# Kernel tuning notes

Hardware: AMD Instinct MI355X
Metric: run time of the kernel (lower is better)

The kernel has to match this reference:

```python
import jax, jax.numpy as jnp
import numpy as np

SCALE = 4
D_MODEL = 128   # in_channels // scale
D_STATE = 16
D_CONV = 4
D_INNER = 256   # expand * d_model
DT_RANK = 8     # ceil(d_model / 16)


def setup_inputs() -> dict:
    key = jax.random.key(0)
    ks = jax.random.split(key, 10)
    B, C, H, W = 4, 512, 48, 48
    s = 0.02
    x = jax.random.normal(ks[0], (B, C, H, W), jnp.float32)
    in_proj_w = jax.random.normal(ks[1], (SCALE, 2 * D_INNER, D_MODEL), jnp.float32) * s
    conv_w = jax.random.normal(ks[2], (SCALE, D_INNER, D_CONV), jnp.float32) * s
    conv_b = jax.random.normal(ks[3], (SCALE, D_INNER), jnp.float32) * s
    x_proj_w = jax.random.normal(ks[4], (SCALE, DT_RANK + 2 * D_STATE, D_INNER), jnp.float32) * s
    dt_proj_w = jax.random.normal(ks[5], (SCALE, D_INNER, DT_RANK), jnp.float32) * s
    dt_proj_b = jax.random.uniform(ks[6], (SCALE, D_INNER), jnp.float32, 0.001, 0.1)
    A_log = jnp.broadcast_to(jnp.log(jnp.arange(1, D_STATE + 1, dtype=jnp.float32)), (SCALE, D_INNER, D_STATE)).copy()
    D = jnp.ones((SCALE, D_INNER), jnp.float32)
    out_proj_w = jax.random.normal(ks[7], (SCALE, D_MODEL, D_INNER), jnp.float32) * s
    return {"x": x, "in_proj_w": in_proj_w, "conv_w": conv_w, "conv_b": conv_b,
            "x_proj_w": x_proj_w, "dt_proj_w": dt_proj_w, "dt_proj_b": dt_proj_b,
            "A_log": A_log, "D": D, "out_proj_w": out_proj_w}


def _mamba(u, Wi, wc, bc, Wx, Wdt, bdt, A_log, Dp, Wo):
    # u: (B, L, d_model)
    B, L, _ = u.shape
    di, n, dtr, dc = Wo.shape[1], A_log.shape[1], Wdt.shape[1], wc.shape[1]
    xz = u @ Wi.T                                   # (B, L, 2*di)
    xp, z = jnp.split(xz, 2, axis=-1)
    # causal depthwise conv along L
    xc = jax.lax.conv_general_dilated(xp.transpose(0, 2, 1), wc[:, None, :], (1,),
                                      [(dc - 1, 0)], feature_group_count=di)
    xs = jax.nn.silu(xc + bc[None, :, None]).transpose(0, 2, 1)  # (B, L, di)
    dbc = xs @ Wx.T
    dt, Bm, Cm = dbc[..., :dtr], dbc[..., dtr:dtr + n], dbc[..., dtr + n:]
    delta = jax.nn.softplus(dt @ Wdt.T + bdt)       # (B, L, di)
    A = -jnp.exp(A_log)                             # (di, n)
    dA = jnp.exp(jnp.einsum('bld,dn->bldn', delta, A))
    dBu = jnp.einsum('bld,bln->bldn', delta * xs, Bm)

    def step(h, inp):
        dA_t, dBu_t, C_t = inp
        h = dA_t * h + dBu_t                        # (B, di, n)
        return h, jnp.einsum('bdn,bn->bd', h, C_t)

    h0 = jnp.zeros((B, di, n), u.dtype)
    _, ys = jax.lax.scan(step, h0, (dA.transpose(1, 0, 2, 3), dBu.transpose(1, 0, 2, 3), Cm.transpose(1, 0, 2)))
    y = ys.transpose(1, 0, 2) + xs * Dp             # (B, L, di)
    y = y * jax.nn.silu(z)
    return y @ Wo.T                                 # (B, L, d_model)


def _cdgf(x_i, x_m):
    fused_global = jnp.maximum(x_i, x_m)
    w_local = jax.nn.sigmoid(jnp.mean(x_i, axis=(2, 3), keepdims=True))
    w_global = jax.nn.sigmoid(jnp.mean(fused_global, axis=(2, 3), keepdims=True))
    return w_local * x_i + w_global * fused_global


def reference(x, in_proj_w, conv_w, conv_b, x_proj_w, dt_proj_w, dt_proj_b, A_log, D, out_proj_w):
    b, c, h, w = x.shape
    cs = c // SCALE
    spx = jnp.split(x, SCALE, axis=1)
    prev = None
    feats = []
    for i in range(SCALE):
        x_i = spx[i] + prev if prev is not None else spx[i]
        sp = x_i.reshape(b, cs, h * w).transpose(0, 2, 1)
        xm = _mamba(sp, in_proj_w[i], conv_w[i], conv_b[i], x_proj_w[i], dt_proj_w[i],
                    dt_proj_b[i], A_log[i], D[i], out_proj_w[i])
        x_m = xm.transpose(0, 2, 1).reshape(b, cs, h, w)
        fused = _cdgf(x_i, x_m)
        feats.append(fused)
        prev = fused
    return jnp.concatenate(feats, axis=1)
```

## Files before the change

### kernel.cpp

```cpp
#include <hip/hip_runtime.h>
#include <cstddef>

#define BB 4
#define LSEQ 2304
#define NST 16
#define NC2 144
#define XSS 264
#define VTS 136

typedef __attribute__((ext_vector_type(8))) short bf16x8;
typedef __attribute__((ext_vector_type(4))) float f32x4;

__device__ __forceinline__ unsigned short f2bf(float f) {
    return (unsigned short)(__float_as_uint(f) >> 16);
}
__device__ __forceinline__ float bf2f(unsigned short u) {
    return __uint_as_float(((unsigned)u) << 16);
}
__device__ __forceinline__ float softplusf(float a) {
    float t = __expf(-fabsf(a));
    return fmaxf(a, 0.f) + __logf(1.f + t);
}
__device__ __forceinline__ float sigm(float a) {
    return 1.f / (1.f + __expf(-a));
}
#define RLS (1.f / (float)LSEQ)
__device__ __forceinline__ void powtree(float e, float* ep) {
    ep[0] = e;
    ep[1] = e * e;
    ep[2] = ep[1] * e;
    ep[3] = ep[1] * ep[1];
    ep[4] = ep[3] * ep[0];
    ep[5] = ep[3] * ep[1];
    ep[6] = ep[3] * ep[2];
    ep[7] = ep[3] * ep[3];
    ep[8] = ep[7] * ep[0];
    ep[9] = ep[7] * ep[1];
    ep[10] = ep[7] * ep[2];
    ep[11] = ep[7] * ep[3];
    ep[12] = ep[7] * ep[4];
    ep[13] = ep[7] * ep[5];
    ep[14] = ep[7] * ep[6];
    ep[15] = ep[7] * ep[7];
}

__device__ __forceinline__ void gate_chain(const float* __restrict__ xsum, const float* __restrict__ fgsum,
                                           int bc, int scale, float& wlv, float& wgv) {
    float sxi = xsum[bc];
    wlv = sigm(sxi * RLS);
    for (int j = 0; j < scale - 1; ++j) {
        float fg = fgsum[j * 512 + bc];
        float wgj = sigm(fg * RLS);
        sxi = xsum[(j + 1) * 512 + bc] + wlv * sxi + wgj * fg;
        wlv = sigm(sxi * RLS);
    }
    wgv = sigm(fgsum[(scale - 1) * 512 + bc] * RLS);
}

__global__ __launch_bounds__(256) void k_init(const float* __restrict__ x,
                                              const float* __restrict__ Wi, const float* __restrict__ Wx,
                                              const float* __restrict__ Wo,
                                              float* __restrict__ xsum, float* __restrict__ fgsum,
                                              unsigned short* __restrict__ Wi_b,
                                              unsigned short* __restrict__ Wx_b,
                                              unsigned short* __restrict__ Wo_b) {
    int vb = blockIdx.x;
    if (vb >= 2048) {
        if (vb == 2048) {
            for (int k = threadIdx.x; k < 2048; k += 256) fgsum[k] = 0.f;
        }
        int i = (vb - 2048) * 256 + threadIdx.x;
        if (i < 262144) { Wi_b[i] = f2bf(Wi[i]); return; }
        int j = i - 262144;
        if (j < 40960) { Wx_b[j] = f2bf(Wx[j]); return; }
        int k = j - 40960;
        if (k < 131072) Wo_b[k] = f2bf(Wo[k]);
        return;
    }
    int s = vb >> 9, bc = vb & 511;
    int b = bc >> 7, c = bc & 127;
    const float* src = x + ((size_t)(b * 512 + s * 128 + c)) * LSEQ;
    float sum = 0.f;
    for (int l = threadIdx.x; l < LSEQ; l += 256) sum += src[l];
    __shared__ float red[256];
    red[threadIdx.x] = sum;
    __syncthreads();
    for (int ss = 128; ss > 0; ss >>= 1) {
        if (threadIdx.x < ss) red[threadIdx.x] += red[threadIdx.x + ss];
        __syncthreads();
    }
    if (threadIdx.x == 0) xsum[s * 512 + bc] = red[0];
}

__global__ __launch_bounds__(256) void k_convx(const float* __restrict__ x,
                                               const float* __restrict__ xip, int xipbs,
                                               float* __restrict__ xiout,
                                               const float* __restrict__ xmT, float* __restrict__ out,
                                               const float* __restrict__ xsum, const float* __restrict__ fgsum,
                                               const unsigned short* __restrict__ Wib,
                                               const float* __restrict__ wc, const float* __restrict__ bcv,
                                               const unsigned short* __restrict__ Wx,
                                               const float* __restrict__ Wdt, const float* __restrict__ bdt,
                                               unsigned short* __restrict__ xsb,
                                               unsigned short* __restrict__ zb,
                                               float* __restrict__ dbc,
                                               float* __restrict__ Pq, float* __restrict__ Sb,
                                               int scale) {
    __shared__ __align__(16) char uni[19 * VTS * sizeof(unsigned short)];
    unsigned short* vtile = (unsigned short*)uni;
    float (*dbc_lds)[52] = (float (*)[52])uni;
    __shared__ unsigned short xp[19 * XSS];
    __shared__ unsigned short z_lds[16 * 256];
    __shared__ unsigned short xs_lds[16 * XSS];
    int tid = threadIdx.x;
    int wave = tid >> 6, lane = tid & 63;
    int b = blockIdx.y;
    int l0 = blockIdx.x * 16;
    size_t rowbase = (size_t)b * LSEQ + l0;
    int row = lane & 15, kq = lane >> 4;
    int cr = (lane >> 4) * 4, cc = lane & 15;

    {
        int cl = tid >> 4, ll = tid & 15;
        if (scale == 0) {
            #pragma unroll
            for (int co = 0; co < 8; ++co) {
                int c = co * 16 + cl;
                float v = x[((size_t)(b * 512 + c)) * LSEQ + l0 + ll];
                vtile[(ll + 3) * VTS + c] = f2bf(v);
            }
            if (tid < 128) {
                int c = tid;
                if (l0 > 0) {
                    float4 x4 = *(const float4*)(x + ((size_t)(b * 512 + c)) * LSEQ + l0 - 4);
                    vtile[0 * VTS + c] = f2bf(x4.y);
                    vtile[1 * VTS + c] = f2bf(x4.z);
                    vtile[2 * VTS + c] = f2bf(x4.w);
                } else {
                    vtile[0 * VTS + c] = 0;
                    vtile[1 * VTS + c] = 0;
                    vtile[2 * VTS + c] = 0;
                }
            }
        } else {
            #pragma unroll
            for (int co = 0; co < 8; ++co) {
                int c = co * 16 + cl;
                int bc = b * 128 + c;
                float wlv, wgv;
                gate_chain(xsum, fgsum, bc, scale, wlv, wgv);
                int rl = l0 + ll;
                float xi = xip[((size_t)(b * xipbs + c)) * LSEQ + rl];
                float xm = xmT[((size_t)bc) * LSEQ + rl];
                float o = wlv * xi + wgv * fmaxf(xi, xm);
                float v = x[((size_t)(b * 512 + scale * 128 + c)) * LSEQ + rl] + o;
                out[((size_t)(b * 512 + (scale - 1) * 128 + c)) * LSEQ + rl] = o;
                xiout[((size_t)bc) * LSEQ + rl] = v;
                vtile[(ll + 3) * VTS + c] = f2bf(v);
            }
            if (tid < 128) {
                int c = tid;
                int bc = b * 128 + c;
                if (l0 > 0) {
                    float wlv, wgv;
                    gate_chain(xsum, fgsum, bc, scale, wlv, wgv);
                    float4 xi4 = *(const float4*)(xip + ((size_t)(b * xipbs + c)) * LSEQ + l0 - 4);
                    float4 xm4 = *(const float4*)(xmT + ((size_t)bc) * LSEQ + l0 - 4);
                    float4 xn4 = *(const float4*)(x + ((size_t)(b * 512 + scale * 128 + c)) * LSEQ + l0 - 4);
                    vtile[0 * VTS + c] = f2bf(xn4.y + wlv * xi4.y + wgv * fmaxf(xi4.y, xm4.y));
                    vtile[1 * VTS + c] = f2bf(xn4.z + wlv * xi4.z + wgv * fmaxf(xi4.z, xm4.z));
                    vtile[2 * VTS + c] = f2bf(xn4.w + wlv * xi4.w + wgv * fmaxf(xi4.w, xm4.w));
                } else {
                    vtile[0 * VTS + c] = 0;
                    vtile[1 * VTS + c] = 0;
                    vtile[2 * VTS + c] = 0;
                }
            }
        }
    }
    __syncthreads();

    bf16x8 A0[4], A1[4];
    #pragma unroll
    for (int k = 0; k < 4; ++k) {
        A0[k] = *(const bf16x8*)&vtile[row * VTS + k * 32 + kq * 8];
        A1[k] = *(const bf16x8*)&vtile[(row + 3) * VTS + k * 32 + kq * 8];
    }
    #pragma unroll
    for (int t = 0; t < 4; ++t) {
        int j = wave * 4 + t;
        bf16x8 Bt[4];
        #pragma unroll
        for (int k = 0; k < 4; ++k)
            Bt[k] = *(const bf16x8*)(Wib + (size_t)(j * 16 + row) * 128 + k * 32 + kq * 8);
        f32x4 acc0 = (f32x4){0.f, 0.f, 0.f, 0.f};
        f32x4 acc1 = (f32x4){0.f, 0.f, 0.f, 0.f};
        #pragma unroll
        for (int k = 0; k < 4; ++k) {
            acc0 = __builtin_amdgcn_mfma_f32_16x16x32_bf16(A0[k], Bt[k], acc0, 0, 0, 0);
            acc1 = __builtin_amdgcn_mfma_f32_16x16x32_bf16(A1[k], Bt[k], acc1, 0, 0, 0);
        }
        #pragma unroll
        for (int r = 0; r < 4; ++r)
            xp[(cr + r) * XSS + j * 16 + cc] = f2bf(acc0[r]);
        #pragma unroll
        for (int r = 0; r < 4; ++r) {
            int t_ = cr + r;
            if (t_ >= 13) xp[(t_ + 3) * XSS + j * 16 + cc] = f2bf(acc1[r]);
        }
    }
    #pragma unroll
    for (int t = 0; t < 4; ++t) {
        int j = 16 + wave * 4 + t;
        bf16x8 Bt[4];
        #pragma unroll
        for (int k = 0; k < 4; ++k)
            Bt[k] = *(const bf16x8*)(Wib + (size_t)(j * 16 + row) * 128 + k * 32 + kq * 8);
        f32x4 acc = (f32x4){0.f, 0.f, 0.f, 0.f};
        #pragma unroll
        for (int k = 0; k < 4; ++k)
            acc = __builtin_amdgcn_mfma_f32_16x16x32_bf16(A1[k], Bt[k], acc, 0, 0, 0);
        #pragma unroll
        for (int r = 0; r < 4; ++r)
            z_lds[(cr + r) * 256 + (j - 16) * 16 + cc] = f2bf(acc[r]);
    }
    __syncthreads();

    int d = tid;
    #pragma unroll
    for (int it = 0; it < 2; ++it) {
        int zr = (tid >> 5) + it * 8, zs = tid & 31;
        *(bf16x8*)(zb + (rowbase + zr) * 256 + zs * 8) = *(const bf16x8*)&z_lds[zr * 256 + zs * 8];
    }
    float w0 = wc[d * 4 + 0], w1 = wc[d * 4 + 1], w2 = wc[d * 4 + 2], w3 = wc[d * 4 + 3];
    float bc = bcv[d];
    #pragma unroll
    for (int li = 0; li < 16; ++li) {
        float acc = bc + w0 * bf2f(xp[li * XSS + d]) + w1 * bf2f(xp[(li + 1) * XSS + d])
                       + w2 * bf2f(xp[(li + 2) * XSS + d]) + w3 * bf2f(xp[(li + 3) * XSS + d]);
        float v = acc / (1.f + __expf(-acc));
        xs_lds[li * XSS + d] = f2bf(v);
    }
    __syncthreads();

    #pragma unroll
    for (int it = 0; it < 2; ++it) {
        int zr = (tid >> 5) + it * 8, zs = tid & 31;
        *(bf16x8*)(xsb + (rowbase + zr) * 256 + zs * 8) = *(const bf16x8*)&xs_lds[zr * XSS + zs * 8];
    }
    if (wave < 3) {
        f32x4 acc = (f32x4){0.f, 0.f, 0.f, 0.f};
        int n = wave * 16 + row;
        #pragma unroll
        for (int k0 = 0; k0 < 256; k0 += 32) {
            bf16x8 af = *(const bf16x8*)&xs_lds[row * XSS + k0 + kq * 8];
            bf16x8 bfr;
            if (n < 40) bfr = *(const bf16x8*)(Wx + (size_t)n * 256 + k0 + kq * 8);
            else        bfr = (bf16x8){0, 0, 0, 0, 0, 0, 0, 0};
            acc = __builtin_amdgcn_mfma_f32_16x16x32_bf16(af, bfr, acc, 0, 0, 0);
        }
        int nn = wave * 16 + cc;
        #pragma unroll
        for (int r = 0; r < 4; ++r)
            dbc_lds[cr + r][nn] = acc[r];
    }
    __syncthreads();

    if (tid < 160) {
        int fi = tid * 4;
        int r0 = fi / 40, c0 = fi % 40;
        float4 v = make_float4(dbc_lds[r0][c0], dbc_lds[r0][c0 + 1], dbc_lds[r0][c0 + 2], dbc_lds[r0][c0 + 3]);
        ((float4*)(dbc + rowbase * 40))[tid] = v;
    }
    float wdt[8];
    #pragma unroll
    for (int j = 0; j < 8; ++j) wdt[j] = Wdt[d * 8 + j];
    float bd = bdt[d];
    float S[NST];
    #pragma unroll
    for (int n = 0; n < NST; ++n) S[n] = 0.f;
    float sdv = 0.f;
    #pragma unroll
    for (int li = 0; li < 16; ++li) {
        float dt0 = bd, dt1 = 0.f;
        #pragma unroll
        for (int j = 0; j < 4; ++j) {
            dt0 += dbc_lds[li][j] * wdt[j];
            dt1 += dbc_lds[li][4 + j] * wdt[4 + j];
        }
        float dv = softplusf(dt0 + dt1);
        sdv += dv;
        float e = __expf(-dv);
        float du = dv * bf2f(xs_lds[li * XSS + d]);
        float ep[16];
        powtree(e, ep);
        #pragma unroll
        for (int n = 0; n < NST; ++n)
            S[n] = ep[n] * S[n] + du * dbc_lds[li][8 + n];
    }
    size_t cb = (size_t)(b * NC2 + blockIdx.x);
    Pq[cb * 256 + d] = sdv;
    #pragma unroll
    for (int n = 0; n < NST; ++n) Sb[(cb * NST + n) * 256 + d] = S[n];
}

__global__ __launch_bounds__(256) void k_scan2(const float* __restrict__ Pq, float* __restrict__ Sb) {
    int t = blockIdx.x * 256 + threadIdx.x;
    int b = t >> 12, n = (t >> 8) & 15, d = t & 255;
    float np1 = (float)(n + 1);
    size_t pq0 = (size_t)b * NC2 * 256 + d;
    size_t sb0 = ((size_t)b * NC2 * NST + n) * 256 + d;
    float h = 0.f;
    float sdv[4], S[4];
    #pragma unroll
    for (int j = 0; j < 4; ++j) {
        sdv[j] = Pq[pq0 + (size_t)j * 256];
        S[j]   = Sb[sb0 + (size_t)j * NST * 256];
    }
    for (int c0 = 0; c0 < NC2; c0 += 4) {
        float nsdv[4], nS[4];
        if (c0 + 4 < NC2) {
            #pragma unroll
            for (int j = 0; j < 4; ++j) {
                nsdv[j] = Pq[pq0 + (size_t)(c0 + 4 + j) * 256];
                nS[j]   = Sb[sb0 + (size_t)(c0 + 4 + j) * NST * 256];
            }
        }
        #pragma unroll
        for (int j = 0; j < 4; ++j) {
            float qp = __expf(-np1 * sdv[j]);
            Sb[sb0 + (size_t)(c0 + j) * NST * 256] = h;
            h = qp * h + S[j];
        }
        #pragma unroll
        for (int j = 0; j < 4; ++j) { sdv[j] = nsdv[j]; S[j] = nS[j]; }
    }
}

__global__ __launch_bounds__(256) void k_scan3o(const unsigned short* __restrict__ xsb,
                                                const float* __restrict__ dbc,
                                                const float* __restrict__ Wdt, const float* __restrict__ bdt,
                                                const float* __restrict__ Dp, const unsigned short* __restrict__ zb,
                                                const float* __restrict__ Sb,
                                                const unsigned short* __restrict__ Wob,
                                                float* __restrict__ xmT,
                                                const float* __restrict__ xi_ptr, int xibs,
                                                float* __restrict__ fgs) {
    __shared__ float dblds[16][40];
    __shared__ unsigned short y_lds[16 * XSS];
    int d = threadIdx.x;
    int wave = d >> 6, lane = d & 63;
    int c = blockIdx.x, b = blockIdx.y;
    int l0 = c * 16;
    size_t rowbase = (size_t)b * LSEQ + l0;
    if (d < 160) ((float4*)&dblds[0][0])[d] = ((const float4*)(dbc + rowbase * 40))[d];
    float wdt[8];
    #pragma unroll
    for (int j = 0; j < 8; ++j) wdt[j] = Wdt[d * 8 + j];
    float bd = bdt[d];
    size_t cb = (size_t)(b * NC2 + c);
    float h[NST];
    #pragma unroll
    for (int n = 0; n < NST; ++n) h[n] = Sb[(cb * NST + n) * 256 + d];
    float Dv = Dp[d];
    __syncthreads();
    #pragma unroll
    for (int li = 0; li < 16; ++li) {
        size_t row = rowbase + li;
        float dt0 = bd, dt1 = 0.f;
        #pragma unroll
        for (int j = 0; j < 4; ++j) {
            dt0 += dblds[li][j] * wdt[j];
            dt1 += dblds[li][4 + j] * wdt[4 + j];
        }
        float dv = softplusf(dt0 + dt1);
        float xv = bf2f(xsb[row * 256 + d]);
        float e = __expf(-dv);
        float du = dv * xv;
        float ep[16];
        powtree(e, ep);
        float y0 = 0.f, y1 = 0.f, y2 = 0.f, y3 = 0.f;
        #pragma unroll
        for (int n = 0; n < NST; n += 4) {
            h[n]     = ep[n]     * h[n]     + du * dblds[li][8 + n];
            h[n + 1] = ep[n + 1] * h[n + 1] + du * dblds[li][9 + n];
            h[n + 2] = ep[n + 2] * h[n + 2] + du * dblds[li][10 + n];
            h[n + 3] = ep[n + 3] * h[n + 3] + du * dblds[li][11 + n];
            y0 += h[n] * dblds[li][24 + n];
            y1 += h[n + 1] * dblds[li][25 + n];
            y2 += h[n + 2] * dblds[li][26 + n];
            y3 += h[n + 3] * dblds[li][27 + n];
        }
        float y = (y0 + y1) + (y2 + y3);
        float z = bf2f(zb[row * 256 + d]);
        float sz = z / (1.f + __expf(-z));
        y_lds[li * XSS + d] = f2bf((y + xv * Dv) * sz);
    }
    __syncthreads();

    int row = lane & 15, kq = lane >> 4;
    int cr = (lane >> 4) * 4, cc = lane & 15;
    #pragma unroll
    for (int t = 0; t < 2; ++t) {
        int j = wave * 2 + t;
        f32x4 acc = (f32x4){0.f, 0.f, 0.f, 0.f};
        #pragma unroll
        for (int k0 = 0; k0 < 256; k0 += 32) {
            bf16x8 af = *(const bf16x8*)&y_lds[row * XSS + k0 + kq * 8];
            bf16x8 bfr = *(const bf16x8*)(Wob + (size_t)(j * 16 + row) * 256 + k0 + kq * 8);
            acc = __builtin_amdgcn_mfma_f32_16x16x32_bf16(af, bfr, acc, 0, 0, 0);
        }
        float4 v = make_float4(acc[0], acc[1], acc[2], acc[3]);
        *(float4*)(xmT + ((size_t)(b * 128 + j * 16 + cc)) * LSEQ + l0 + cr) = v;
        const float* xi_p = xi_ptr + ((size_t)(b * xibs + j * 16 + cc)) * LSEQ + l0 + cr;
        float4 xiv = *(const float4*)xi_p;
        float p = fmaxf(xiv.x, acc[0]) + fmaxf(xiv.y, acc[1]) + fmaxf(xiv.z, acc[2]) + fmaxf(xiv.w, acc[3]);
        p += __shfl_down(p, 32);
        p += __shfl_down(p, 16);
        if (lane < 16) atomicAdd(&fgs[b * 128 + j * 16 + lane], p);
    }
}

__global__ __launch_bounds__(256) void k_fin(const float* __restrict__ xi1, const float* __restrict__ xmT,
                                             const float* __restrict__ xsum, const float* __restrict__ fgsum,
                                             float* __restrict__ out) {
    int bc = blockIdx.x;
    int b = bc >> 7, c = bc & 127;
    float wlv, wgv;
    gate_chain(xsum, fgsum, bc, 4, wlv, wgv);
    const float4* xi_p = (const float4*)(xi1 + (size_t)bc * LSEQ);
    const float4* xm_p = (const float4*)(xmT + (size_t)bc * LSEQ);
    float4* out_p = (float4*)(out + ((size_t)(b * 512 + 384 + c)) * LSEQ);
    #pragma unroll
    for (int it = 0; it < 3; ++it) {
        int idx = threadIdx.x + it * 256;
        if (idx < 576) {
            float4 xi = xi_p[idx], xm = xm_p[idx];
            float4 o;
            o.x = wlv * xi.x + wgv * fmaxf(xi.x, xm.x);
            o.y = wlv * xi.y + wgv * fmaxf(xi.y, xm.y);
            o.z = wlv * xi.z + wgv * fmaxf(xi.z, xm.z);
            o.w = wlv * xi.w + wgv * fmaxf(xi.w, xm.w);
            out_p[idx] = o;
        }
    }
}

extern "C" void kernel_launch(void* const* d_in, const int* in_sizes, int n_in,
                              void* d_out, int out_size, void* d_ws, size_t ws_size,
                              hipStream_t stream) {
    const float* x    = (const float*)d_in[0];
    const float* Wi   = (const float*)d_in[1];
    const float* wc   = (const float*)d_in[2];
    const float* bcv  = (const float*)d_in[3];
    const float* Wx   = (const float*)d_in[4];
    const float* Wdt  = (const float*)d_in[5];
    const float* bdt  = (const float*)d_in[6];
    const float* Dp   = (const float*)d_in[8];
    const float* Wo   = (const float*)d_in[9];
    float* out = (float*)d_out;
    float* w = (float*)d_ws;

    float* xsum  = w;
    float* fgsum = xsum + 2048;
    float* xiA   = fgsum + 2048;
    float* xiB   = xiA + 1179648;
    float* dbc   = xiB + 1179648;
    float* Pq    = dbc + 368640;
    float* Sb    = Pq + 147456;
    float* xmT   = Sb + 2359296;
    unsigned short* zb    = (unsigned short*)(xmT + 1179648);
    unsigned short* xs_b  = zb + 2359296;
    unsigned short* Wi_b  = xs_b + 2359296;
    unsigned short* Wx_b  = Wi_b + 262144;
    unsigned short* Wo_b  = Wx_b + 40960;

    k_init<<<2048 + 1696, 256, 0, stream>>>(x, Wi, Wx, Wo, xsum, fgsum, Wi_b, Wx_b, Wo_b);

    float* xi_buf[2] = { xiA, xiB };
    for (int i = 0; i < 4; ++i) {
        const float* wc_i   = wc   + (size_t)i * 256 * 4;
        const float* bc_i   = bcv  + (size_t)i * 256;
        const float* Wdt_i  = Wdt  + (size_t)i * 256 * 8;
        const float* bdt_i  = bdt  + (size_t)i * 256;
        const float* D_i    = Dp   + (size_t)i * 256;
        const unsigned short* Wi_bi = Wi_b + (size_t)i * 512 * 128;
        const unsigned short* Wx_bi = Wx_b + (size_t)i * 40 * 256;
        const unsigned short* Wo_bi = Wo_b + (size_t)i * 128 * 256;

        const float* xip = (i <= 1) ? x : xi_buf[(i - 1) & 1];
        int xipbs = (i <= 1) ? 512 : 128;
        const float* xisc = (i == 0) ? x : xi_buf[i & 1];
        int xiscbs = (i == 0) ? 512 : 128;

        k_convx<<<dim3(NC2, BB), 256, 0, stream>>>(x, xip, xipbs, xi_buf[i & 1], xmT, out,
                                                   xsum, fgsum, Wi_bi, wc_i, bc_i, Wx_bi,
                                                   Wdt_i, bdt_i, xs_b, zb, dbc, Pq, Sb, i);
        k_scan2<<<64, 256, 0, stream>>>(Pq, Sb);
        k_scan3o<<<dim3(NC2, BB), 256, 0, stream>>>(xs_b, dbc, Wdt_i, bdt_i, D_i, zb, Sb, Wo_bi, xmT,
                                                    xisc, xiscbs, fgsum + (size_t)i * 512);
    }
    k_fin<<<512, 256, 0, stream>>>(xi_buf[1], xmT, xsum, fgsum, out);
}
```

Before: 277.9 us.

## Fuse inter-chunk scan into output kernel with a global atomic barrier

Removes the separate k_scan2 launch and runs the cross-chunk state propagation inside the first 64 blocks of k_scan3o. Every block then spins on a per-stage atomic counter until those 64 blocks finish, after which it reads the propagated states. This saves one kernel launch and its gap per stage. It relies on all 576 blocks being co-resident, or at least on the first 64 being scheduled, so a different scheduling order could deadlock. The spin-wait also keeps the waiting blocks idle.

New measurement: 476.3 us. 71.4% more time.

```diff
diff --git a/kernel.cpp b/kernel.cpp
--- a/kernel.cpp
+++ b/kernel.cpp
@@ -61,6 +61,7 @@
                                               const float* __restrict__ Wi, const float* __restrict__ Wx,
                                               const float* __restrict__ Wo,
                                               float* __restrict__ xsum, float* __restrict__ fgsum,
+                                              int* __restrict__ done,
                                               unsigned short* __restrict__ Wi_b,
                                               unsigned short* __restrict__ Wx_b,
                                               unsigned short* __restrict__ Wo_b) {
@@ -68,6 +69,7 @@
     if (vb >= 2048) {
         if (vb == 2048) {
             for (int k = threadIdx.x; k < 2048; k += 256) fgsum[k] = 0.f;
+            if (threadIdx.x < 16) done[threadIdx.x] = 0;
         }
         int i = (vb - 2048) * 256 + threadIdx.x;
         if (i < 262144) { Wi_b[i] = f2bf(Wi[i]); return; }
@@ -304,48 +306,15 @@
     for (int n = 0; n < NST; ++n) Sb[(cb * NST + n) * 256 + d] = S[n];
 }
 
-__global__ __launch_bounds__(256) void k_scan2(const float* __restrict__ Pq, float* __restrict__ Sb) {
-    int t = blockIdx.x * 256 + threadIdx.x;
-    int b = t >> 12, n = (t >> 8) & 15, d = t & 255;
-    float np1 = (float)(n + 1);
-    size_t pq0 = (size_t)b * NC2 * 256 + d;
-    size_t sb0 = ((size_t)b * NC2 * NST + n) * 256 + d;
-    float h = 0.f;
-    float sdv[4], S[4];
-    #pragma unroll
-    for (int j = 0; j < 4; ++j) {
-        sdv[j] = Pq[pq0 + (size_t)j * 256];
-        S[j]   = Sb[sb0 + (size_t)j * NST * 256];
-    }
-    for (int c0 = 0; c0 < NC2; c0 += 4) {
-        float nsdv[4], nS[4];
-        if (c0 + 4 < NC2) {
-            #pragma unroll
-            for (int j = 0; j < 4; ++j) {
-                nsdv[j] = Pq[pq0 + (size_t)(c0 + 4 + j) * 256];
-                nS[j]   = Sb[sb0 + (size_t)(c0 + 4 + j) * NST * 256];
-            }
-        }
-        #pragma unroll
-        for (int j = 0; j < 4; ++j) {
-            float qp = __expf(-np1 * sdv[j]);
-            Sb[sb0 + (size_t)(c0 + j) * NST * 256] = h;
-            h = qp * h + S[j];
-        }
-        #pragma unroll
-        for (int j = 0; j < 4; ++j) { sdv[j] = nsdv[j]; S[j] = nS[j]; }
-    }
-}
-
 __global__ __launch_bounds__(256) void k_scan3o(const unsigned short* __restrict__ xsb,
                                                 const float* __restrict__ dbc,
                                                 const float* __restrict__ Wdt, const float* __restrict__ bdt,
                                                 const float* __restrict__ Dp, const unsigned short* __restrict__ zb,
-                                                const float* __restrict__ Sb,
+                                                const float* __restrict__ Pq, float* __restrict__ Sb,
                                                 const unsigned short* __restrict__ Wob,
                                                 float* __restrict__ xmT,
                                                 const float* __restrict__ xi_ptr, int xibs,
-                                                float* __restrict__ fgs) {
+                                                float* __restrict__ fgs, int* __restrict__ done) {
     __shared__ float dblds[16][40];
     __shared__ unsigned short y_lds[16 * XSS];
     int d = threadIdx.x;
@@ -358,11 +327,54 @@
     #pragma unroll
     for (int j = 0; j < 8; ++j) wdt[j] = Wdt[d * 8 + j];
     float bd = bdt[d];
+    float Dv = Dp[d];
+
+    int flat = blockIdx.y * NC2 + blockIdx.x;
+    if (flat < 64) {
+        int t = flat * 256 + d;
+        int b2 = t >> 12, n2 = (t >> 8) & 15, d2 = t & 255;
+        float np1 = (float)(n2 + 1);
+        size_t pq0 = (size_t)b2 * NC2 * 256 + d2;
+        size_t sb0 = ((size_t)b2 * NC2 * NST + n2) * 256 + d2;
+        float h = 0.f;
+        float sdv[4], S[4];
+        #pragma unroll
+        for (int j = 0; j < 4; ++j) {
+            sdv[j] = Pq[pq0 + (size_t)j * 256];
+            S[j]   = Sb[sb0 + (size_t)j * NST * 256];
+        }
+        for (int c0 = 0; c0 < NC2; c0 += 4) {
+            float nsdv[4], nS[4];
+            if (c0 + 4 < NC2) {
+                #pragma unroll
+                for (int j = 0; j < 4; ++j) {
+                    nsdv[j] = Pq[pq0 + (size_t)(c0 + 4 + j) * 256];
+                    nS[j]   = Sb[sb0 + (size_t)(c0 + 4 + j) * NST * 256];
+                }
+            }
+            #pragma unroll
+            for (int j = 0; j < 4; ++j) {
+                float qp = __expf(-np1 * sdv[j]);
+                Sb[sb0 + (size_t)(c0 + j) * NST * 256] = h;
+                h = qp * h + S[j];
+            }
+            #pragma unroll
+            for (int j = 0; j < 4; ++j) { sdv[j] = nsdv[j]; S[j] = nS[j]; }
+        }
+        __threadfence();
+    }
+    __syncthreads();
+    if (d == 0) {
+        if (flat < 64) atomicAdd(done, 1);
+        while (atomicAdd(done, 0) < 64) __builtin_amdgcn_s_sleep(16);
+    }
+    __syncthreads();
+    __threadfence();
+
     size_t cb = (size_t)(b * NC2 + c);
     float h[NST];
     #pragma unroll
     for (int n = 0; n < NST; ++n) h[n] = Sb[(cb * NST + n) * 256 + d];
-    float Dv = Dp[d];
     __syncthreads();
     #pragma unroll
     for (int li = 0; li < 16; ++li) {
@@ -463,7 +475,8 @@
 
     float* xsum  = w;
     float* fgsum = xsum + 2048;
-    float* xiA   = fgsum + 2048;
+    int*   dcnt  = (int*)(fgsum + 2048);
+    float* xiA   = fgsum + 2048 + 16;
     float* xiB   = xiA + 1179648;
     float* dbc   = xiB + 1179648;
     float* Pq    = dbc + 368640;
@@ -475,7 +488,7 @@
     unsigned short* Wx_b  = Wi_b + 262144;
     unsigned short* Wo_b  = Wx_b + 40960;
 
-    k_init<<<2048 + 1696, 256, 0, stream>>>(x, Wi, Wx, Wo, xsum, fgsum, Wi_b, Wx_b, Wo_b);
+    k_init<<<2048 + 1696, 256, 0, stream>>>(x, Wi, Wx, Wo, xsum, fgsum, dcnt, Wi_b, Wx_b, Wo_b);
 
     float* xi_buf[2] = { xiA, xiB };
     for (int i = 0; i < 4; ++i) {
@@ -496,9 +509,8 @@
         k_convx<<<dim3(NC2, BB), 256, 0, stream>>>(x, xip, xipbs, xi_buf[i & 1], xmT, out,
                                                    xsum, fgsum, Wi_bi, wc_i, bc_i, Wx_bi,
                                                    Wdt_i, bdt_i, xs_b, zb, dbc, Pq, Sb, i);
-        k_scan2<<<64, 256, 0, stream>>>(Pq, Sb);
-        k_scan3o<<<dim3(NC2, BB), 256, 0, stream>>>(xs_b, dbc, Wdt_i, bdt_i, D_i, zb, Sb, Wo_bi, xmT,
-                                                    xisc, xiscbs, fgsum + (size_t)i * 512);
+        k_scan3o<<<dim3(NC2, BB), 256, 0, stream>>>(xs_b, dbc, Wdt_i, bdt_i, D_i, zb, Pq, Sb, Wo_bi, xmT,
+                                                    xisc, xiscbs, fgsum + (size_t)i * 512, dcnt + i);
     }
     k_fin<<<512, 256, 0, stream>>>(xi_buf[1], xmT, xsum, fgsum, out);
 }
```
